# Kernel tuning notes

Measured on AMD Instinct MI355X. Metric: run time of the kernel, lower is better.

## Reference

```python
import jax, jax.numpy as jnp
import numpy as np

N = 50000      # nodes
E = 800000     # edges (avg degree 16)
IN = 128       # in_dim
OUT = 128      # out_dim
K = 4          # Chebyshev order
NEIG = 64      # num_eigs
H = 128        # eigval_hidden_dim
BN_EPS = 1e-5


def setup_inputs() -> dict:
    key = jax.random.key(0)
    ks = jax.random.split(key, 12)
    feature = jax.random.normal(ks[0], (N, IN), jnp.float32)
    # linear over concat of (K Chebyshev blocks + 1 spectral block) = (K+1)*IN
    lin_w = jax.random.normal(ks[1], ((K + 1) * IN, OUT), jnp.float32) / np.sqrt((K + 1) * IN)
    lin_b = jnp.zeros((OUT,), jnp.float32)
    # eigval_filter MLP: 1 -> H -> H -> 1 (ReLU between)
    ew0 = jax.random.normal(ks[2], (1, H), jnp.float32)
    eb0 = jnp.zeros((H,), jnp.float32)
    ew1 = jax.random.normal(ks[3], (H, H), jnp.float32) / np.sqrt(H)
    eb1 = jnp.zeros((H,), jnp.float32)
    ew2 = jax.random.normal(ks[4], (H, 1), jnp.float32) / np.sqrt(H)
    eb2 = jnp.zeros((1,), jnp.float32)
    bn_gamma = jnp.ones((OUT,), jnp.float32)
    bn_beta = jnp.zeros((OUT,), jnp.float32)
    lambda_max = jnp.ones((1,), jnp.float32)
    # cached (detached) spectral data for the graph
    evecs = jax.random.normal(ks[5], (N, NEIG), jnp.float32)
    evals = jax.random.uniform(ks[6], (NEIG,), jnp.float32)
    edge_src = jax.random.randint(ks[7], (E,), 0, N, jnp.int32).astype(jnp.int64)
    edge_dst = jax.random.randint(ks[8], (E,), 0, N, jnp.int32).astype(jnp.int64)
    return dict(feature=feature, lin_w=lin_w, lin_b=lin_b, ew0=ew0, eb0=eb0,
                ew1=ew1, eb1=eb1, ew2=ew2, eb2=eb2, bn_gamma=bn_gamma,
                bn_beta=bn_beta, lambda_max=lambda_max, evecs=evecs,
                evals=evals, edge_src=edge_src, edge_dst=edge_dst)


def reference(feature, lin_w, lin_b, ew0, eb0, ew1, eb1, ew2, eb2,
              bn_gamma, bn_beta, lambda_max, evecs, evals, edge_src, edge_dst):
    src = edge_src.astype(jnp.int32)
    dst = edge_dst.astype(jnp.int32)
    # in-degrees (messages arrive at dst) and D^-1/2, clamped at 1
    deg = jax.ops.segment_sum(jnp.ones((E,), jnp.float32), dst, num_segments=N)
    d_sqrt = jnp.clip(deg, 1.0, None) ** -0.5  # [N]
    d_sqrt = d_sqrt[:, None]                   # [N,1]

    def unn_laplacian(x):
        m = (x * d_sqrt)[src]                              # [E,IN]
        agg = jax.ops.segment_sum(m, dst, num_segments=N)  # [N,IN]
        return agg * d_sqrt

    re_norm = 2.0 / lambda_max  # broadcast scalar (per-node in dgl, constant here)

    X0 = feature
    blocks = [X0]
    h = unn_laplacian(X0)
    X1 = -re_norm * h + X0 * (re_norm - 1.0)
    blocks.append(X1)
    for _ in range(2, K):
        h = unn_laplacian(X1)
        Xi = -2.0 * re_norm * h + X1 * 2.0 * (re_norm - 1.0) - X0
        blocks.append(Xi)
        X1, X0 = Xi, X1

    # spectral filtering: evecs^T f, scale by MLP(evals), project back
    z = jax.nn.relu(evals[:, None] @ ew0 + eb0)   # [NEIG,H]
    z = jax.nn.relu(z @ ew1 + eb1)                # [NEIG,H]
    ef = z @ ew2 + eb2                            # [NEIG,1]
    hs = jnp.einsum('ne,nf->ef', evecs, feature)  # [NEIG,IN]
    hs = ef * hs
    hs = jnp.einsum('ne,ef->nf', evecs, hs)       # [N,IN]
    blocks.append(hs)

    Xt = jnp.concatenate(blocks, axis=1)          # [N,(K+1)*IN]
    out = Xt @ lin_w + lin_b                      # [N,OUT]

    # BatchNorm1d (training-mode batch statistics, biased variance)
    mu = jnp.mean(out, axis=0)
    var = jnp.mean((out - mu) ** 2, axis=0)
    out = (out - mu) * jax.lax.rsqrt(var + BN_EPS) * bn_gamma + bn_beta
    out = jax.nn.relu(out)
    # dropout p=0.0 -> identity; residual disabled
    return out
```

## Files before the change

### kernel.cpp

```cpp
#include <hip/hip_runtime.h>

#define N_NODES 50000
#define N_EDGES 800000
#define IN_F    128
#define OUT_F   128
#define NEIG    64
#define HDIM    128
#define BN_EPSF 1e-5f
#define XB_ROWS 50048
#define XB_COLS 640
#define SCAN_BLK 49
#define HSP_BLOCKS 521
#define HSP_NODES 96
#define RED_CHUNK 33
#define N_REP 8

typedef __attribute__((ext_vector_type(8))) short short8;
typedef __attribute__((ext_vector_type(4))) float floatx4;

#define OFF_XB      0
#define OFF_X1F     (XB_ROWS * XB_COLS / 2)
#define OFF_X2F     (OFF_X1F + N_NODES * IN_F)
#define OFF_WT      (OFF_X2F + N_NODES * IN_F)
#define OFF_DSQRT   (OFF_WT + 40960)
#define OFF_HS      (OFF_DSQRT + N_NODES)
#define OFF_EF      (OFF_HS + NEIG * OUT_F)
#define OFF_COLSUM  (OFF_EF + NEIG)
#define OFF_COLSQ   (OFF_COLSUM + OUT_F)
#define OFF_DEG     (OFF_COLSQ + OUT_F)
#define OFF_ROWSTART (OFF_DEG + N_REP * N_NODES)
#define OFF_CSR     (OFF_ROWSTART + N_NODES + 1)
#define OFF_BSUM    (OFF_CSR + N_EDGES)
#define OFF_RANK    (OFF_BSUM + 64)
#define OFF_RS4     (OFF_RANK + N_EDGES)

static __device__ inline unsigned short f2bf(float f) {
    union { float f; unsigned int u; } v; v.f = f;
    unsigned int r = (v.u + 0x7FFFu + ((v.u >> 16) & 1u)) >> 16;
    return (unsigned short)r;
}
static __device__ inline float bf2f(unsigned int u16) {
    union { unsigned int u; float f; } v; v.u = u16 << 16;
    return v.f;
}

__global__ __launch_bounds__(256) void k_prep(const float* __restrict__ feat,
                                              const float* __restrict__ W,
                                              unsigned short* __restrict__ Xb,
                                              unsigned short* __restrict__ Wt,
                                              int* __restrict__ degR,
                                              float* __restrict__ small) {
    int b = blockIdx.x;
    if (b < 3125) {
        int t = b * 256 + threadIdx.x;
        int n = t >> 4, c8 = (t & 15) * 8;
        float4 a = *(const float4*)&feat[n * IN_F + c8];
        float4 bb = *(const float4*)&feat[n * IN_F + c8 + 4];
        ushort4 o0, o1;
        o0.x = f2bf(a.x); o0.y = f2bf(a.y); o0.z = f2bf(a.z); o0.w = f2bf(a.w);
        o1.x = f2bf(bb.x); o1.y = f2bf(bb.y); o1.z = f2bf(bb.z); o1.w = f2bf(bb.w);
        *(ushort4*)&Xb[(size_t)n * XB_COLS + c8]     = o0;
        *(ushort4*)&Xb[(size_t)n * XB_COLS + c8 + 4] = o1;
    } else if (b < 3445) {
        int t = (b - 3125) * 256 + threadIdx.x;
        int k = t >> 7, n = t & 127;
        Wt[n * 640 + k] = f2bf(W[k * 128 + n]);
    } else {
        int i = (b - 3445) * 256 + threadIdx.x;
        if (i < N_REP * N_NODES) degR[i] = 0;
        if (i < NEIG * OUT_F + NEIG + 2 * OUT_F) small[i] = 0.0f;
    }
}

__global__ __launch_bounds__(256) void k_stage2(const float* __restrict__ evecs,
                                                const float* __restrict__ feat,
                                                float* __restrict__ partials,
                                                const float* __restrict__ evals,
                                                const float* __restrict__ ew0,
                                                const float* __restrict__ eb0,
                                                const float* __restrict__ ew1,
                                                const float* __restrict__ eb1,
                                                const float* __restrict__ ew2,
                                                const float* __restrict__ eb2,
                                                float* __restrict__ ef,
                                                int* __restrict__ degR,
                                                const int* __restrict__ dst,
                                                int* __restrict__ rank) {
    int b = blockIdx.x;
    int t = threadIdx.x;
    if (b < HSP_BLOCKS) {
        __shared__ float sEv[32 * NEIG];
        __shared__ float sFt[32 * IN_F];
        int e0 = (t >> 5) * 8;
        int f0 = (t & 31) * 4;
        float acc[8][4];
#pragma unroll
        for (int r = 0; r < 8; ++r)
#pragma unroll
            for (int c = 0; c < 4; ++c) acc[r][c] = 0.0f;

        int n0 = b * HSP_NODES;
        for (int ch = 0; ch < HSP_NODES; ch += 32) {
            int base = n0 + ch;
            {
                int r = t >> 3, c = (t & 7) * 8;
                int n = base + r;
                float4 a, bb;
                if (n < N_NODES) {
                    a = *(const float4*)&evecs[(size_t)n * NEIG + c];
                    bb = *(const float4*)&evecs[(size_t)n * NEIG + c + 4];
                } else {
                    a = make_float4(0, 0, 0, 0); bb = a;
                }
                *(float4*)&sEv[r * NEIG + c] = a;
                *(float4*)&sEv[r * NEIG + c + 4] = bb;
            }
            {
                int r = t >> 3, c = (t & 7) * 16;
                int n = base + r;
#pragma unroll
                for (int q = 0; q < 4; ++q) {
                    float4 v = (n < N_NODES) ? *(const float4*)&feat[(size_t)n * IN_F + c + q * 4]
                                             : make_float4(0, 0, 0, 0);
                    *(float4*)&sFt[r * IN_F + c + q * 4] = v;
                }
            }
            __syncthreads();
#pragma unroll 2
            for (int i = 0; i < 32; ++i) {
                float4 ev0 = *(float4*)&sEv[i * NEIG + e0];
                float4 ev1 = *(float4*)&sEv[i * NEIG + e0 + 4];
                float4 fv  = *(float4*)&sFt[i * IN_F + f0];
                float evv[8] = {ev0.x, ev0.y, ev0.z, ev0.w, ev1.x, ev1.y, ev1.z, ev1.w};
#pragma unroll
                for (int r = 0; r < 8; ++r) {
                    acc[r][0] += evv[r] * fv.x;
                    acc[r][1] += evv[r] * fv.y;
                    acc[r][2] += evv[r] * fv.z;
                    acc[r][3] += evv[r] * fv.w;
                }
            }
            __syncthreads();
        }
        float* p = &partials[(size_t)b * (NEIG * IN_F)];
#pragma unroll
        for (int r = 0; r < 8; ++r)
            *(float4*)&p[(e0 + r) * IN_F + f0] = make_float4(acc[r][0], acc[r][1], acc[r][2], acc[r][3]);
    } else if (b < HSP_BLOCKS + 32) {
        __shared__ float z0[2][HDIM];
        __shared__ float red[2][HDIM];
        int sub = t >> 7, j = t & 127;
        int i = (b - HSP_BLOCKS) * 2 + sub;
        float ev = evals[i];
        z0[sub][j] = fmaxf(0.0f, ev * ew0[j] + eb0[j]);
        __syncthreads();
        float s0 = 0.f, s1 = 0.f, s2 = 0.f, s3 = 0.f;
        for (int h = 0; h < HDIM; h += 4) {
            s0 += z0[sub][h]     * ew1[(h) * HDIM + j];
            s1 += z0[sub][h + 1] * ew1[(h + 1) * HDIM + j];
            s2 += z0[sub][h + 2] * ew1[(h + 2) * HDIM + j];
            s3 += z0[sub][h + 3] * ew1[(h + 3) * HDIM + j];
        }
        float z1 = fmaxf(0.0f, eb1[j] + s0 + s1 + s2 + s3);
        red[sub][j] = z1 * ew2[j];
        __syncthreads();
        for (int off = 64; off > 0; off >>= 1) {
            if (j < off) red[sub][j] += red[sub][j + off];
            __syncthreads();
        }
        if (j == 0) ef[i] = red[sub][0] + eb2[0];
    } else {
        int e = (b - (HSP_BLOCKS + 32)) * 256 + t;
        if (e < N_EDGES) {
            int rep = e & (N_REP - 1);
            rank[e] = atomicAdd(&degR[rep * N_NODES + dst[e]], 1);
        }
    }
}

__global__ __launch_bounds__(1024) void k_stage3(int* __restrict__ degR,
                                                 int* __restrict__ row_start,
                                                 int* __restrict__ bsum,
                                                 const float* __restrict__ partials,
                                                 float* __restrict__ hs_small) {
    int b = blockIdx.x;
    int t = threadIdx.x;
    if (b < SCAN_BLK) {
        __shared__ int sd[1024];
        int i = b * 1024 + t;
        int d0 = 0, d1 = 0, d2 = 0, d3 = 0, d4 = 0, d5 = 0, d6 = 0, d7 = 0;
        if (i < N_NODES) {
            d0 = degR[i];
            d1 = degR[N_NODES + i];
            d2 = degR[2 * N_NODES + i];
            d3 = degR[3 * N_NODES + i];
            d4 = degR[4 * N_NODES + i];
            d5 = degR[5 * N_NODES + i];
            d6 = degR[6 * N_NODES + i];
            d7 = degR[7 * N_NODES + i];
        }
        int total = d0 + d1 + d2 + d3 + d4 + d5 + d6 + d7;
        sd[t] = total;
        __syncthreads();
        for (int off = 1; off < 1024; off <<= 1) {
            int v = (t >= off) ? sd[t - off] : 0;
            __syncthreads();
            sd[t] += v;
            __syncthreads();
        }
        if (i < N_NODES) {
            row_start[i] = sd[t] - total;
            degR[i] = total;
            int p = d0;
            degR[N_NODES + i] = p;     p += d1;
            degR[2 * N_NODES + i] = p; p += d2;
            degR[3 * N_NODES + i] = p; p += d3;
            degR[4 * N_NODES + i] = p; p += d4;
            degR[5 * N_NODES + i] = p; p += d5;
            degR[6 * N_NODES + i] = p; p += d6;
            degR[7 * N_NODES + i] = p;
        }
        if (t == 1023) bsum[b] = sd[1023];
    } else {
        int b2 = b - SCAN_BLK;
        int grp = b2 & 7;
        int chunk = b2 >> 3;
        int idx = grp * 1024 + t;
        int j0 = chunk * RED_CHUNK;
        int j1 = min(j0 + RED_CHUNK, HSP_BLOCKS);
        float s = 0.0f;
        for (int j = j0; j < j1; ++j) s += partials[(size_t)j * (NEIG * IN_F) + idx];
        atomicAdd(&hs_small[idx], s);
    }
}

__global__ void k_scan2(int* __restrict__ bsum) {
    int t = threadIdx.x;
    int orig = (t < SCAN_BLK) ? bsum[t] : 0;
    int v = orig;
    for (int off = 1; off < 64; off <<= 1) {
        int u = __shfl_up(v, off);
        if (t >= off) v += u;
    }
    if (t < SCAN_BLK) bsum[t] = v - orig;
}

__global__ __launch_bounds__(1024) void k_scan3(const int* __restrict__ degR,
                                                int* __restrict__ row_start,
                                                const int* __restrict__ bsum,
                                                float* __restrict__ dsq,
                                                int* __restrict__ rs4) {
    int i = blockIdx.x * 1024 + threadIdx.x;
    if (i < N_NODES) {
        int r = row_start[i] + bsum[blockIdx.x];
        row_start[i] = r;
        rs4[i] = r;
#pragma unroll
        for (int rep = 1; rep < N_REP; ++rep)
            rs4[rep * N_NODES + i] = r + degR[rep * N_NODES + i];
        dsq[i] = rsqrtf((float)max(degR[i], 1));
    }
    if (i == 0) row_start[N_NODES] = N_EDGES;
}

__global__ __launch_bounds__(256) void k_stage6(const int* __restrict__ src,
                                                const int* __restrict__ dst,
                                                const int* __restrict__ rank,
                                                const int* __restrict__ rs4,
                                                int* __restrict__ csr_src,
                                                unsigned short* __restrict__ Xb,
                                                const float* __restrict__ evecs,
                                                const float* __restrict__ hs_small,
                                                const float* __restrict__ ef) {
    int b = blockIdx.x;
    int t = threadIdx.x;
    if (b < 3125) {
        int e = b * 256 + t;
        if (e < N_EDGES) {
            int rep = e & (N_REP - 1);
            csr_src[rs4[rep * N_NODES + dst[e]] + rank[e]] = src[e];
        }
    } else {
        __shared__ float sShs[NEIG * HDIM];
        __shared__ float sEv[32 * NEIG];
        int n0 = (b - 3125) * 32;
        {
            float efv = ef[t >> 2];
            int pbase = t * 32;
#pragma unroll
            for (int q = 0; q < 8; ++q) {
                float4 v = *(const float4*)&hs_small[pbase + q * 4];
                v.x *= efv; v.y *= efv; v.z *= efv; v.w *= efv;
                *(float4*)&sShs[pbase + q * 4] = v;
            }
        }
        {
            int r = t >> 3, c = (t & 7) * 8;
            int n = n0 + r;
            float4 a, bb;
            if (n < N_NODES) {
                a = *(const float4*)&evecs[(size_t)n * NEIG + c];
                bb = *(const float4*)&evecs[(size_t)n * NEIG + c + 4];
            } else {
                a = make_float4(0, 0, 0, 0); bb = a;
            }
            *(float4*)&sEv[r * NEIG + c] = a;
            *(float4*)&sEv[r * NEIG + c + 4] = bb;
        }
        __syncthreads();
        int nb = (t >> 5) * 4;
        int f0 = (t & 31) * 4;
        float acc[4][4];
#pragma unroll
        for (int q = 0; q < 4; ++q)
#pragma unroll
            for (int c = 0; c < 4; ++c) acc[q][c] = 0.0f;
        for (int e = 0; e < NEIG; ++e) {
            float4 sv = *(float4*)&sShs[e * HDIM + f0];
#pragma unroll
            for (int q = 0; q < 4; ++q) {
                float evv = sEv[(nb + q) * NEIG + e];
                acc[q][0] += evv * sv.x;
                acc[q][1] += evv * sv.y;
                acc[q][2] += evv * sv.z;
                acc[q][3] += evv * sv.w;
            }
        }
#pragma unroll
        for (int q = 0; q < 4; ++q) {
            int n = n0 + nb + q;
            if (n < N_NODES) {
                ushort4 o;
                o.x = f2bf(acc[q][0]); o.y = f2bf(acc[q][1]);
                o.z = f2bf(acc[q][2]); o.w = f2bf(acc[q][3]);
                *(ushort4*)&Xb[(size_t)n * XB_COLS + 4 * IN_F + f0] = o;
            }
        }
    }
}

__global__ __launch_bounds__(256) void k_gather(const int* __restrict__ row_start,
                                                const int* __restrict__ csr_src,
                                                const float* __restrict__ dsq,
                                                const unsigned short* __restrict__ srcb,
                                                const unsigned short* __restrict__ prevb,
                                                const unsigned short* __restrict__ ppb,
                                                unsigned short* __restrict__ outb,
                                                const float* __restrict__ lm, int first) {
    int n = (blockIdx.x * 256 + threadIdx.x) >> 6;
    int lane = threadIdx.x & 63;
    if (n >= N_NODES) return;
    float rn = 2.0f / lm[0];
    float ax = 0.0f, ay = 0.0f;
    int beg = row_start[n], end = row_start[n + 1];
    int i = beg;
    for (; i + 16 <= end; i += 16) {
        int s[16]; float c[16]; unsigned int p[16];
#pragma unroll
        for (int j = 0; j < 16; ++j) s[j] = __builtin_amdgcn_readfirstlane(csr_src[i + j]);
#pragma unroll
        for (int j = 0; j < 16; ++j) c[j] = dsq[s[j]];
#pragma unroll
        for (int j = 0; j < 16; ++j)
            p[j] = *(const unsigned int*)&srcb[(size_t)s[j] * XB_COLS + lane * 2];
#pragma unroll
        for (int j = 0; j < 16; ++j) {
            ax += c[j] * bf2f(p[j] & 0xffffu);
            ay += c[j] * bf2f(p[j] >> 16);
        }
    }
    for (; i + 8 <= end; i += 8) {
        int s[8]; float c[8]; unsigned int p[8];
#pragma unroll
        for (int j = 0; j < 8; ++j) s[j] = __builtin_amdgcn_readfirstlane(csr_src[i + j]);
#pragma unroll
        for (int j = 0; j < 8; ++j) c[j] = dsq[s[j]];
#pragma unroll
        for (int j = 0; j < 8; ++j)
            p[j] = *(const unsigned int*)&srcb[(size_t)s[j] * XB_COLS + lane * 2];
#pragma unroll
        for (int j = 0; j < 8; ++j) {
            ax += c[j] * bf2f(p[j] & 0xffffu);
            ay += c[j] * bf2f(p[j] >> 16);
        }
    }
    for (; i + 4 <= end; i += 4) {
        int s[4]; float c[4]; unsigned int p[4];
#pragma unroll
        for (int j = 0; j < 4; ++j) s[j] = __builtin_amdgcn_readfirstlane(csr_src[i + j]);
#pragma unroll
        for (int j = 0; j < 4; ++j) c[j] = dsq[s[j]];
#pragma unroll
        for (int j = 0; j < 4; ++j)
            p[j] = *(const unsigned int*)&srcb[(size_t)s[j] * XB_COLS + lane * 2];
#pragma unroll
        for (int j = 0; j < 4; ++j) {
            ax += c[j] * bf2f(p[j] & 0xffffu);
            ay += c[j] * bf2f(p[j] >> 16);
        }
    }
    for (; i < end; ++i) {
        int s = __builtin_amdgcn_readfirstlane(csr_src[i]);
        float sc = dsq[s];
        unsigned int pv = *(const unsigned int*)&srcb[(size_t)s * XB_COLS + lane * 2];
        ax += sc * bf2f(pv & 0xffffu);
        ay += sc * bf2f(pv >> 16);
    }
    float ds = dsq[n];
    float a = (first ? -rn : -2.0f * rn) * ds;
    float b = first ? (rn - 1.0f) : 2.0f * (rn - 1.0f);
    unsigned int pu = *(const unsigned int*)&prevb[(size_t)n * XB_COLS + lane * 2];
    float rx = a * ax + b * bf2f(pu & 0xffffu);
    float ry = a * ay + b * bf2f(pu >> 16);
    if (ppb) {
        unsigned int qu = *(const unsigned int*)&ppb[(size_t)n * XB_COLS + lane * 2];
        rx -= bf2f(qu & 0xffffu);
        ry -= bf2f(qu >> 16);
    }
    unsigned int packed = (unsigned int)f2bf(rx) | ((unsigned int)f2bf(ry) << 16);
    *(unsigned int*)&outb[(size_t)n * XB_COLS + lane * 2] = packed;
}

__global__ __launch_bounds__(256) void k_gemm(const unsigned short* __restrict__ Xb,
                                              const unsigned short* __restrict__ Wt,
                                              const float* __restrict__ bias,
                                              float* __restrict__ out,
                                              float* __restrict__ colsum,
                                              float* __restrict__ colsq) {
    __shared__ unsigned short sA[128 * 32];
    __shared__ unsigned short sB[128 * 32];
    __shared__ float cs[4][OUT_F];
    __shared__ float cq[4][OUT_F];
    int tid = threadIdx.x;
    int wave = tid >> 6, lane = tid & 63;
    int quad = lane >> 4, m16 = lane & 15;
    int row0 = blockIdx.x * 128;

    floatx4 acc[2][8];
#pragma unroll
    for (int mt = 0; mt < 2; ++mt)
#pragma unroll
        for (int nt = 0; nt < 8; ++nt) acc[mt][nt] = (floatx4)(0.0f);

    int r  = tid >> 2;
    int c8 = (tid & 3) * 8;
    int gr0 = min(row0 + r, N_NODES - 1);
    int gr1 = min(row0 + r + 64, N_NODES - 1);

    for (int k0 = 0; k0 < 640; k0 += 32) {
        *(uint4*)&sA[r * 32 + c8]        = *(const uint4*)&Xb[(size_t)gr0 * XB_COLS + k0 + c8];
        *(uint4*)&sA[(r + 64) * 32 + c8] = *(const uint4*)&Xb[(size_t)gr1 * XB_COLS + k0 + c8];
        *(uint4*)&sB[r * 32 + c8]        = *(const uint4*)&Wt[r * 640 + k0 + c8];
        *(uint4*)&sB[(r + 64) * 32 + c8] = *(const uint4*)&Wt[(r + 64) * 640 + k0 + c8];
        __syncthreads();
        short8 a0 = *(short8*)&sA[(wave * 32 + m16) * 32 + quad * 8];
        short8 a1 = *(short8*)&sA[(wave * 32 + 16 + m16) * 32 + quad * 8];
#pragma unroll
        for (int nt = 0; nt < 8; ++nt) {
            short8 b = *(short8*)&sB[(nt * 16 + m16) * 32 + quad * 8];
            acc[0][nt] = __builtin_amdgcn_mfma_f32_16x16x32_bf16(a0, b, acc[0][nt], 0, 0, 0);
            acc[1][nt] = __builtin_amdgcn_mfma_f32_16x16x32_bf16(a1, b, acc[1][nt], 0, 0, 0);
        }
        __syncthreads();
    }
#pragma unroll
    for (int nt = 0; nt < 8; ++nt) {
        int col = nt * 16 + m16;
        float bb = bias[col];
        float sv = 0.0f, sq = 0.0f;
#pragma unroll
        for (int mt = 0; mt < 2; ++mt) {
            int rbase = row0 + wave * 32 + mt * 16 + quad * 4;
#pragma unroll
            for (int reg = 0; reg < 4; ++reg) {
                int row = rbase + reg;
                if (row < N_NODES) {
                    float w = acc[mt][nt][reg] + bb;
                    out[(size_t)row * OUT_F + col] = w;
                    sv += w;
                    sq += w * w;
                }
            }
        }
        sv += __shfl_down(sv, 32); sq += __shfl_down(sq, 32);
        sv += __shfl_down(sv, 16); sq += __shfl_down(sq, 16);
        if (lane < 16) { cs[wave][col] = sv; cq[wave][col] = sq; }
    }
    __syncthreads();
    if (tid < OUT_F) {
        float s = cs[0][tid] + cs[1][tid] + cs[2][tid] + cs[3][tid];
        float q = cq[0][tid] + cq[1][tid] + cq[2][tid] + cq[3][tid];
        atomicAdd(&colsum[tid], s);
        atomicAdd(&colsq[tid], q);
    }
}

__global__ void k_bn_apply(float* __restrict__ out, const float* __restrict__ colsum,
                           const float* __restrict__ colsq, const float* __restrict__ gamma,
                           const float* __restrict__ beta) {
    int t = blockIdx.x * 256 + threadIdx.x;
    int n = t >> 5, c = t & 31;
    float4 v = *(float4*)&out[n * OUT_F + c * 4];
    float4 s = *(const float4*)&colsum[c * 4];
    float4 q = *(const float4*)&colsq[c * 4];
    float4 g = *(const float4*)&gamma[c * 4];
    float4 b = *(const float4*)&beta[c * 4];
    const float invN = 1.0f / (float)N_NODES;
    float mux = s.x * invN, muy = s.y * invN, muz = s.z * invN, muw = s.w * invN;
    float ix = rsqrtf(q.x * invN - mux * mux + BN_EPSF);
    float iy = rsqrtf(q.y * invN - muy * muy + BN_EPSF);
    float iz = rsqrtf(q.z * invN - muz * muz + BN_EPSF);
    float iw = rsqrtf(q.w * invN - muw * muw + BN_EPSF);
    v.x = fmaxf(0.0f, (v.x - mux) * ix * g.x + b.x);
    v.y = fmaxf(0.0f, (v.y - muy) * iy * g.y + b.y);
    v.z = fmaxf(0.0f, (v.z - muz) * iz * g.z + b.z);
    v.w = fmaxf(0.0f, (v.w - muw) * iw * g.w + b.w);
    *(float4*)&out[n * OUT_F + c * 4] = v;
}

extern "C" void kernel_launch(void* const* d_in, const int* in_sizes, int n_in,
                              void* d_out, int out_size, void* d_ws, size_t ws_size,
                              hipStream_t stream) {
    const float* feature    = (const float*)d_in[0];
    const float* lin_w      = (const float*)d_in[1];
    const float* lin_b      = (const float*)d_in[2];
    const float* ew0        = (const float*)d_in[3];
    const float* eb0        = (const float*)d_in[4];
    const float* ew1        = (const float*)d_in[5];
    const float* eb1        = (const float*)d_in[6];
    const float* ew2        = (const float*)d_in[7];
    const float* eb2        = (const float*)d_in[8];
    const float* bn_gamma   = (const float*)d_in[9];
    const float* bn_beta    = (const float*)d_in[10];
    const float* lambda_max = (const float*)d_in[11];
    const float* evecs      = (const float*)d_in[12];
    const float* evals      = (const float*)d_in[13];
    const int*   edge_src   = (const int*)d_in[14];
    const int*   edge_dst   = (const int*)d_in[15];

    float* out = (float*)d_out;
    float* ws  = (float*)d_ws;
    unsigned short* Xb = (unsigned short*)(ws + OFF_XB);
    unsigned short* Wt = (unsigned short*)(ws + OFF_WT);
    float* dsq      = ws + OFF_DSQRT;
    float* hs_small = ws + OFF_HS;
    float* ef       = ws + OFF_EF;
    float* colsum   = ws + OFF_COLSUM;
    float* colsq    = ws + OFF_COLSQ;
    int*   degR     = (int*)(ws + OFF_DEG);
    int*   row_start= (int*)(ws + OFF_ROWSTART);
    int*   csr_src  = (int*)(ws + OFF_CSR);
    int*   bsum     = (int*)(ws + OFF_BSUM);
    int*   rank     = (int*)(ws + OFF_RANK);
    int*   rs4      = (int*)(ws + OFF_RS4);
    float* partials = ws + OFF_X1F;

    k_prep<<<5008, 256, 0, stream>>>(feature, lin_w, Xb, Wt, degR, hs_small);

    k_stage2<<<HSP_BLOCKS + 32 + 3125, 256, 0, stream>>>(evecs, feature, partials,
                                                         evals, ew0, eb0, ew1, eb1, ew2, eb2,
                                                         ef, degR, edge_dst, rank);

    k_stage3<<<SCAN_BLK + 128, 1024, 0, stream>>>(degR, row_start, bsum, partials, hs_small);
    k_scan2<<<1, 64, 0, stream>>>(bsum);
    k_scan3<<<SCAN_BLK, 1024, 0, stream>>>(degR, row_start, bsum, dsq, rs4);

    k_stage6<<<3125 + 1563, 256, 0, stream>>>(edge_src, edge_dst, rank, rs4, csr_src,
                                              Xb, evecs, hs_small, ef);

    const int GBLK = (N_NODES * 64 + 255) / 256;
    k_gather<<<GBLK, 256, 0, stream>>>(row_start, csr_src, dsq,
                                       Xb + 0, Xb + 0, (const unsigned short*)nullptr,
                                       Xb + IN_F, lambda_max, 1);
    k_gather<<<GBLK, 256, 0, stream>>>(row_start, csr_src, dsq,
                                       Xb + IN_F, Xb + IN_F, Xb + 0,
                                       Xb + 2 * IN_F, lambda_max, 0);
    k_gather<<<GBLK, 256, 0, stream>>>(row_start, csr_src, dsq,
                                       Xb + 2 * IN_F, Xb + 2 * IN_F, Xb + IN_F,
                                       Xb + 3 * IN_F, lambda_max, 0);

    k_gemm<<<(N_NODES + 127) / 128, 256, 0, stream>>>(Xb, Wt, lin_b, out, colsum, colsq);
    k_bn_apply<<<(N_NODES * 32) / 256, 256, 0, stream>>>(out, colsum, colsq, bn_gamma, bn_beta);
}
```

Before: 342.5 us.

## Split gather wave into half-waves, fold block scan into scan3, batch rank atomics

The neighbor gather now processes two edges per wave step, with each half-wave loading 8-byte vectors (4 bf16) per lane. A cross-half shuffle then reduces the partial sums, and only the lower half writes. The separate single-block bsum scan kernel is removed, and each scan3 block recomputes the 49-element prefix itself in one wave. The edge-rank atomic section now handles 8 edges per thread, issuing all loads before the atomics to get more in flight, and the block count is cut to match. The aim is fewer, wider memory requests in the gather and one less kernel launch, in exchange for redundant scan work and some divergence in the tail handling.

```diff
diff --git a/kernel.cpp b/kernel.cpp
--- a/kernel.cpp
+++ b/kernel.cpp
@@ -14,6 +14,7 @@
 #define HSP_NODES 96
 #define RED_CHUNK 33
 #define N_REP 8
+#define RANK_BLOCKS 391
 
 typedef __attribute__((ext_vector_type(8))) short short8;
 typedef __attribute__((ext_vector_type(4))) float floatx4;
@@ -170,10 +171,26 @@
         }
         if (j == 0) ef[i] = red[sub][0] + eb2[0];
     } else {
-        int e = (b - (HSP_BLOCKS + 32)) * 256 + t;
-        if (e < N_EDGES) {
-            int rep = e & (N_REP - 1);
-            rank[e] = atomicAdd(&degR[rep * N_NODES + dst[e]], 1);
+        int bb = b - (HSP_BLOCKS + 32);
+        int base = bb * 2048 + t;
+        int d[8], rk[8];
+#pragma unroll
+        for (int k = 0; k < 8; ++k) {
+            int e = base + k * 256;
+            d[k] = (e < N_EDGES) ? dst[e] : 0;
+        }
+#pragma unroll
+        for (int k = 0; k < 8; ++k) {
+            int e = base + k * 256;
+            if (e < N_EDGES) {
+                int rep = e & (N_REP - 1);
+                rk[k] = atomicAdd(&degR[rep * N_NODES + d[k]], 1);
+            }
+        }
+#pragma unroll
+        for (int k = 0; k < 8; ++k) {
+            int e = base + k * 256;
+            if (e < N_EDGES) rank[e] = rk[k];
         }
     }
 }
@@ -234,25 +251,26 @@
     }
 }
 
-__global__ void k_scan2(int* __restrict__ bsum) {
-    int t = threadIdx.x;
-    int orig = (t < SCAN_BLK) ? bsum[t] : 0;
-    int v = orig;
-    for (int off = 1; off < 64; off <<= 1) {
-        int u = __shfl_up(v, off);
-        if (t >= off) v += u;
-    }
-    if (t < SCAN_BLK) bsum[t] = v - orig;
-}
-
 __global__ __launch_bounds__(1024) void k_scan3(const int* __restrict__ degR,
                                                 int* __restrict__ row_start,
                                                 const int* __restrict__ bsum,
                                                 float* __restrict__ dsq,
                                                 int* __restrict__ rs4) {
-    int i = blockIdx.x * 1024 + threadIdx.x;
+    __shared__ int sOff;
+    int t = threadIdx.x;
+    if (t < 64) {
+        int orig = (t < SCAN_BLK) ? bsum[t] : 0;
+        int v = orig;
+        for (int off = 1; off < 64; off <<= 1) {
+            int u = __shfl_up(v, off);
+            if (t >= off) v += u;
+        }
+        if (t == blockIdx.x) sOff = v - orig;
+    }
+    __syncthreads();
+    int i = blockIdx.x * 1024 + t;
     if (i < N_NODES) {
-        int r = row_start[i] + bsum[blockIdx.x];
+        int r = row_start[i] + sOff;
         row_start[i] = r;
         rs4[i] = r;
 #pragma unroll
@@ -350,75 +368,97 @@
     int n = (blockIdx.x * 256 + threadIdx.x) >> 6;
     int lane = threadIdx.x & 63;
     if (n >= N_NODES) return;
+    int half = lane >> 5;
+    int cb = (lane & 31) * 4;
     float rn = 2.0f / lm[0];
-    float ax = 0.0f, ay = 0.0f;
+    float a0 = 0.f, a1 = 0.f, a2 = 0.f, a3 = 0.f;
     int beg = row_start[n], end = row_start[n + 1];
     int i = beg;
     for (; i + 16 <= end; i += 16) {
-        int s[16]; float c[16]; unsigned int p[16];
+        int s[16]; float c[16]; uint2 p[8];
 #pragma unroll
         for (int j = 0; j < 16; ++j) s[j] = __builtin_amdgcn_readfirstlane(csr_src[i + j]);
 #pragma unroll
         for (int j = 0; j < 16; ++j) c[j] = dsq[s[j]];
 #pragma unroll
-        for (int j = 0; j < 16; ++j)
-            p[j] = *(const unsigned int*)&srcb[(size_t)s[j] * XB_COLS + lane * 2];
-#pragma unroll
-        for (int j = 0; j < 16; ++j) {
-            ax += c[j] * bf2f(p[j] & 0xffffu);
-            ay += c[j] * bf2f(p[j] >> 16);
+        for (int j = 0; j < 8; ++j) {
+            int se = half ? s[2 * j + 1] : s[2 * j];
+            p[j] = *(const uint2*)&srcb[(size_t)se * XB_COLS + cb];
+        }
+#pragma unroll
+        for (int j = 0; j < 8; ++j) {
+            float cc = half ? c[2 * j + 1] : c[2 * j];
+            a0 += cc * bf2f(p[j].x & 0xffffu);
+            a1 += cc * bf2f(p[j].x >> 16);
+            a2 += cc * bf2f(p[j].y & 0xffffu);
+            a3 += cc * bf2f(p[j].y >> 16);
         }
     }
     for (; i + 8 <= end; i += 8) {
-        int s[8]; float c[8]; unsigned int p[8];
+        int s[8]; float c[8]; uint2 p[4];
 #pragma unroll
         for (int j = 0; j < 8; ++j) s[j] = __builtin_amdgcn_readfirstlane(csr_src[i + j]);
 #pragma unroll
         for (int j = 0; j < 8; ++j) c[j] = dsq[s[j]];
 #pragma unroll
-        for (int j = 0; j < 8; ++j)
-            p[j] = *(const unsigned int*)&srcb[(size_t)s[j] * XB_COLS + lane * 2];
-#pragma unroll
-        for (int j = 0; j < 8; ++j) {
-            ax += c[j] * bf2f(p[j] & 0xffffu);
-            ay += c[j] * bf2f(p[j] >> 16);
-        }
-    }
-    for (; i + 4 <= end; i += 4) {
-        int s[4]; float c[4]; unsigned int p[4];
-#pragma unroll
-        for (int j = 0; j < 4; ++j) s[j] = __builtin_amdgcn_readfirstlane(csr_src[i + j]);
-#pragma unroll
-        for (int j = 0; j < 4; ++j) c[j] = dsq[s[j]];
-#pragma unroll
-        for (int j = 0; j < 4; ++j)
-            p[j] = *(const unsigned int*)&srcb[(size_t)s[j] * XB_COLS + lane * 2];
-#pragma unroll
         for (int j = 0; j < 4; ++j) {
-            ax += c[j] * bf2f(p[j] & 0xffffu);
-            ay += c[j] * bf2f(p[j] >> 16);
-        }
-    }
-    for (; i < end; ++i) {
-        int s = __builtin_amdgcn_readfirstlane(csr_src[i]);
-        float sc = dsq[s];
-        unsigned int pv = *(const unsigned int*)&srcb[(size_t)s * XB_COLS + lane * 2];
-        ax += sc * bf2f(pv & 0xffffu);
-        ay += sc * bf2f(pv >> 16);
-    }
+            int se = half ? s[2 * j + 1] : s[2 * j];
+            p[j] = *(const uint2*)&srcb[(size_t)se * XB_COLS + cb];
+        }
+#pragma unroll
+        for (int j = 0; j < 4; ++j) {
+            float cc = half ? c[2 * j + 1] : c[2 * j];
+            a0 += cc * bf2f(p[j].x & 0xffffu);
+            a1 += cc * bf2f(p[j].x >> 16);
+            a2 += cc * bf2f(p[j].y & 0xffffu);
+            a3 += cc * bf2f(p[j].y >> 16);
+        }
+    }
+    for (; i + 2 <= end; i += 2) {
+        int s0 = __builtin_amdgcn_readfirstlane(csr_src[i]);
+        int s1 = __builtin_amdgcn_readfirstlane(csr_src[i + 1]);
+        float c0 = dsq[s0], c1 = dsq[s1];
+        int se = half ? s1 : s0;
+        float cc = half ? c1 : c0;
+        uint2 p = *(const uint2*)&srcb[(size_t)se * XB_COLS + cb];
+        a0 += cc * bf2f(p.x & 0xffffu);
+        a1 += cc * bf2f(p.x >> 16);
+        a2 += cc * bf2f(p.y & 0xffffu);
+        a3 += cc * bf2f(p.y >> 16);
+    }
+    if (i < end) {
+        int s0 = __builtin_amdgcn_readfirstlane(csr_src[i]);
+        float cc = half ? 0.0f : dsq[s0];
+        uint2 p = *(const uint2*)&srcb[(size_t)s0 * XB_COLS + cb];
+        a0 += cc * bf2f(p.x & 0xffffu);
+        a1 += cc * bf2f(p.x >> 16);
+        a2 += cc * bf2f(p.y & 0xffffu);
+        a3 += cc * bf2f(p.y >> 16);
+    }
+    a0 += __shfl_xor(a0, 32);
+    a1 += __shfl_xor(a1, 32);
+    a2 += __shfl_xor(a2, 32);
+    a3 += __shfl_xor(a3, 32);
     float ds = dsq[n];
     float a = (first ? -rn : -2.0f * rn) * ds;
     float b = first ? (rn - 1.0f) : 2.0f * (rn - 1.0f);
-    unsigned int pu = *(const unsigned int*)&prevb[(size_t)n * XB_COLS + lane * 2];
-    float rx = a * ax + b * bf2f(pu & 0xffffu);
-    float ry = a * ay + b * bf2f(pu >> 16);
+    uint2 pu = *(const uint2*)&prevb[(size_t)n * XB_COLS + cb];
+    float r0 = a * a0 + b * bf2f(pu.x & 0xffffu);
+    float r1 = a * a1 + b * bf2f(pu.x >> 16);
+    float r2 = a * a2 + b * bf2f(pu.y & 0xffffu);
+    float r3 = a * a3 + b * bf2f(pu.y >> 16);
     if (ppb) {
-        unsigned int qu = *(const unsigned int*)&ppb[(size_t)n * XB_COLS + lane * 2];
-        rx -= bf2f(qu & 0xffffu);
-        ry -= bf2f(qu >> 16);
-    }
-    unsigned int packed = (unsigned int)f2bf(rx) | ((unsigned int)f2bf(ry) << 16);
-    *(unsigned int*)&outb[(size_t)n * XB_COLS + lane * 2] = packed;
+        uint2 qu = *(const uint2*)&ppb[(size_t)n * XB_COLS + cb];
+        r0 -= bf2f(qu.x & 0xffffu);
+        r1 -= bf2f(qu.x >> 16);
+        r2 -= bf2f(qu.y & 0xffffu);
+        r3 -= bf2f(qu.y >> 16);
+    }
+    if (half == 0) {
+        ushort4 o;
+        o.x = f2bf(r0); o.y = f2bf(r1); o.z = f2bf(r2); o.w = f2bf(r3);
+        *(ushort4*)&outb[(size_t)n * XB_COLS + cb] = o;
+    }
 }
 
 __global__ __launch_bounds__(256) void k_gemm(const unsigned short* __restrict__ Xb,
@@ -557,12 +597,11 @@
 
     k_prep<<<5008, 256, 0, stream>>>(feature, lin_w, Xb, Wt, degR, hs_small);
 
-    k_stage2<<<HSP_BLOCKS + 32 + 3125, 256, 0, stream>>>(evecs, feature, partials,
-                                                         evals, ew0, eb0, ew1, eb1, ew2, eb2,
-                                                         ef, degR, edge_dst, rank);
+    k_stage2<<<HSP_BLOCKS + 32 + RANK_BLOCKS, 256, 0, stream>>>(evecs, feature, partials,
+                                                                evals, ew0, eb0, ew1, eb1, ew2, eb2,
+                                                                ef, degR, edge_dst, rank);
 
     k_stage3<<<SCAN_BLK + 128, 1024, 0, stream>>>(degR, row_start, bsum, partials, hs_small);
-    k_scan2<<<1, 64, 0, stream>>>(bsum);
     k_scan3<<<SCAN_BLK, 1024, 0, stream>>>(degR, row_start, bsum, dsq, rs4);
 
     k_stage6<<<3125 + 1563, 256, 0, stream>>>(edge_src, edge_dst, rank, rs4, csr_src,
```

Result: slower. 892.8 us (+160.7%).
